# Kernel tuning notes

Hardware: AMD Instinct MI355X
Metric: run time of the kernel (lower is better)

The kernel has to match this reference:

```python
import jax, jax.numpy as jnp
import numpy as np
from jax import lax

EPS = 1e-5

def _conv(x, w, stride, padding):
    # x: NCHW, w: OIHW
    return lax.conv_general_dilated(
        x, w, window_strides=(stride, stride), padding=padding,
        dimension_numbers=("NCHW", "OIHW", "NCHW"))

def _bn(x, gamma, beta):
    # BatchNorm2d in training mode: batch statistics over (N, H, W)
    mean = jnp.mean(x, axis=(0, 2, 3), keepdims=True)
    var = jnp.var(x, axis=(0, 2, 3), keepdims=True)
    inv = lax.rsqrt(var + EPS)
    g = gamma.reshape(1, -1, 1, 1)
    b = beta.reshape(1, -1, 1, 1)
    return (x - mean) * inv * g + b

def setup_inputs() -> dict:
    key = jax.random.key(0)
    ks = jax.random.split(key, 5)
    B, Cin, H, W = 128, 64, 56, 56
    Cout = 128
    x = jax.random.normal(ks[0], (B, Cin, H, W), dtype=jnp.float32)
    w1 = jax.random.normal(ks[1], (Cout, Cin, 3, 3), dtype=jnp.float32) * 0.05
    w2 = jax.random.normal(ks[2], (Cout, Cout, 3, 3), dtype=jnp.float32) * 0.05
    wd = jax.random.normal(ks[3], (Cout, Cin, 1, 1), dtype=jnp.float32) * 0.05
    g1 = jnp.ones((Cout,), jnp.float32); b1 = jnp.zeros((Cout,), jnp.float32)
    g2 = jnp.ones((Cout,), jnp.float32); b2 = jnp.zeros((Cout,), jnp.float32)
    gd = jnp.ones((Cout,), jnp.float32); bd = jnp.zeros((Cout,), jnp.float32)
    return {"x": x, "w1": w1, "g1": g1, "b1": b1,
            "w2": w2, "g2": g2, "b2": b2,
            "wd": wd, "gd": gd, "bd": bd}

def reference(x, w1, g1, b1, w2, g2, b2, wd, gd, bd):
    stride = 2
    # conv1 (3x3, stride=2, 'same') -> BN -> ReLU
    out = _conv(x, w1, stride, "SAME")
    out = jax.nn.relu(_bn(out, g1, b1))
    # conv2 (3x3, stride=1, 'same') -> BN
    out = _conv(out, w2, 1, "SAME")
    out = _bn(out, g2, b2)
    # downsample identity: 1x1 conv stride=2 'valid' -> BN
    identity = _bn(_conv(x, wd, stride, "VALID"), gd, bd)
    return jax.nn.relu(out + identity)
```

## Files before the change

kernel.cpp:

```cpp
#include <hip/hip_runtime.h>

constexpr int B = 128, Cin = 64, H = 56, W = 56;
constexpr int Cout = 128, Ho = 28, Wo = 28;
constexpr int HW = Ho * Wo;
constexpr int NPIX = B * HW;
constexpr int NOUT = NPIX * Cout;
constexpr int NBLK2 = NPIX / 256;
constexpr float EPS_ = 1e-5f;
constexpr float CNT_ = (float)NPIX;

constexpr int HPX = 57, WPX = 57;
constexpr int HP1 = 30, WP1 = 30;

typedef __attribute__((ext_vector_type(8))) unsigned short u16x8;
typedef __attribute__((ext_vector_type(4))) unsigned short u16x4;
typedef __attribute__((ext_vector_type(8))) short bf16x8;
typedef __attribute__((ext_vector_type(4))) float f32x4;

__device__ inline float bf2f(unsigned short u) {
    union { unsigned int i; float f; } v; v.i = ((unsigned int)u) << 16; return v.f;
}
__device__ inline unsigned short f2bf(float f) {
    union { float f; unsigned int i; } v; v.f = f;
    return (unsigned short)((v.i + 0x7fffu + ((v.i >> 16) & 1u)) >> 16);
}

__device__ inline void gload16(const void* g, void* l) {
    __builtin_amdgcn_global_load_lds(
        (const __attribute__((address_space(1))) unsigned int*)g,
        (__attribute__((address_space(3))) unsigned int*)l, 16, 0, 0);
}

__global__ __launch_bounds__(512) void k_conv2_mfma(
        const unsigned short* __restrict__ xin,
        const unsigned short* __restrict__ wt,
        unsigned short* __restrict__ yout,
        float* __restrict__ part) {
    constexpr int CIN = 128, WP = 30, KTOT = 1152, NSTEP = 36;
    __shared__ unsigned short Alds[3][256 * 32];
    __shared__ unsigned short Blds[3][128 * 32];
    __shared__ float lsum[8][64], lsq[8][64];
    const int tid = threadIdx.x, w = tid >> 6, l = tid & 63;
    const int wr = w >> 1, wc = w & 1;
    const int bid = (blockIdx.x & 7) * (NBLK2 / 8) + (blockIdx.x >> 3);
    const int p0 = bid * 256;
    const char* xb = (const char*)xin;
    const char* wb = (const char*)wt;

    const int sslot = ((l & 3) ^ ((l >> 3) & 3)) * 16;
    const int rswz  = ((l >> 4) ^ ((l >> 1) & 3)) * 16;

    int gA[2], lofsA[2];
    #pragma unroll
    for (int i = 0; i < 2; ++i) {
        int row = w * 32 + i * 16 + (l >> 2);
        int p = p0 + row;
        int n = p / HW, rr = p % HW;
        int oh = rr / Wo, ow = rr % Wo;
        gA[i] = (((n * HP1 + oh) * WP + ow) * CIN) * 2 + sslot;
        lofsA[i] = row * 64 + (l & 3) * 16;
    }
    const int rowb = w * 16 + (l >> 2);
    const int gB = rowb * KTOT * 2 + sslot;
    const int lofsB = rowb * 64 + (l & 3) * 16;

    f32x4 acc[4][4];
    #pragma unroll
    for (int m = 0; m < 4; ++m)
        #pragma unroll
        for (int n = 0; n < 4; ++n)
            acc[m][n] = (f32x4){0.f, 0.f, 0.f, 0.f};

    gload16(xb + gA[0],      (char*)Alds[0] + lofsA[0]);
    gload16(xb + gA[1],      (char*)Alds[0] + lofsA[1]);
    gload16(wb + gB,         (char*)Blds[0] + lofsB);
    gload16(xb + gA[0] + 64, (char*)Alds[1] + lofsA[0]);
    gload16(xb + gA[1] + 64, (char*)Alds[1] + lofsA[1]);
    gload16(wb + gB + 64,    (char*)Blds[1] + lofsB);

    for (int oi = 0; oi < 3; ++oi) {
        const int Abase = oi * WP * CIN * 2;
        #pragma unroll
        for (int u = 0; u < 12; ++u) {
            const int s = oi * 12 + u;
            const int cur = u % 3;
            if (s + 1 < NSTEP) asm volatile("s_waitcnt vmcnt(3)" ::: "memory");
            else               asm volatile("s_waitcnt vmcnt(0)" ::: "memory");
            __builtin_amdgcn_s_barrier();
            if (s + 2 < NSTEP) {
                const int u2 = u + 2;
                const int j2 = u2 >> 2;
                const int c2 = u2 & 3;
                const int koffA = Abase + (j2 == 3 ? WP * CIN * 2 : j2 * CIN * 2) + c2 * 64;
                const int koffB = (s + 2) * 64;
                const int buf = u2 % 3;
                gload16(xb + gA[0] + koffA, (char*)Alds[buf] + lofsA[0]);
                gload16(xb + gA[1] + koffA, (char*)Alds[buf] + lofsA[1]);
                gload16(wb + gB + koffB,    (char*)Blds[buf] + lofsB);
            }
            bf16x8 bf[4];
            #pragma unroll
            for (int n = 0; n < 4; ++n)
                bf[n] = *(const bf16x8*)((const char*)Blds[cur] + (wc * 64 + n * 16 + (l & 15)) * 64 + rswz);
            #pragma unroll
            for (int m = 0; m < 4; ++m) {
                bf16x8 af = *(const bf16x8*)((const char*)Alds[cur] + (wr * 64 + m * 16 + (l & 15)) * 64 + rswz);
                #pragma unroll
                for (int n = 0; n < 4; ++n)
                    acc[m][n] = __builtin_amdgcn_mfma_f32_16x16x32_bf16(af, bf[n], acc[m][n], 0, 0, 0);
            }
        }
    }

    #pragma unroll
    for (int m = 0; m < 4; ++m) {
        int pq = p0 + wr * 64 + m * 16 + (l >> 4) * 4;
        int n = pq / HW, rr = pq % HW;
        #pragma unroll
        for (int q = 0; q < 4; ++q) {
            int co = wc * 64 + q * 16 + (l & 15);
            u16x4 v;
            #pragma unroll
            for (int r = 0; r < 4; ++r) v[r] = f2bf(acc[m][q][r]);
            *(u16x4*)(yout + ((size_t)(n * Cout + co)) * HW + rr) = v;
        }
    }

    float ps[4], pq_[4];
    #pragma unroll
    for (int n = 0; n < 4; ++n) {
        float s_ = 0.f, q_ = 0.f;
        #pragma unroll
        for (int m = 0; m < 4; ++m)
            #pragma unroll
            for (int r = 0; r < 4; ++r) { float v = acc[m][n][r]; s_ += v; q_ += v * v; }
        s_ += __shfl_xor(s_, 16); q_ += __shfl_xor(q_, 16);
        s_ += __shfl_xor(s_, 32); q_ += __shfl_xor(q_, 32);
        ps[n] = s_; pq_[n] = q_;
    }
    __syncthreads();
    if (l < 16) {
        #pragma unroll
        for (int n = 0; n < 4; ++n) { lsum[w][n * 16 + l] = ps[n]; lsq[w][n * 16 + l] = pq_[n]; }
    }
    __syncthreads();
    if (tid < 128) {
        int c = tid, half = c >> 6, j = c & 63;
        float s_ = 0.f, q_ = 0.f;
        #pragma unroll
        for (int r = 0; r < 4; ++r) { s_ += lsum[r * 2 + half][j]; q_ += lsq[r * 2 + half][j]; }
        part[((size_t)bid * 128 + c) * 2]     = s_;
        part[((size_t)bid * 128 + c) * 2 + 1] = q_;
    }
}

__global__ __launch_bounds__(512) void k_conv1_mfma(
        const unsigned short* __restrict__ xin,
        const unsigned short* __restrict__ wt,
        const unsigned short* __restrict__ wtd,
        unsigned short* __restrict__ yout,
        unsigned short* __restrict__ ydout,
        float* __restrict__ part, float* __restrict__ partd) {
    constexpr int CIN = 64, WP = 57, KTOT = 576, NSTEP = 18;
    __shared__ unsigned short Alds[3][256 * 32];
    __shared__ unsigned short Blds[3][128 * 32];
    __shared__ float lsum[8][64], lsq[8][64];
    const int tid = threadIdx.x, w = tid >> 6, l = tid & 63;
    const int wr = w >> 1, wc = w & 1;
    const int bid = (blockIdx.x & 7) * (NBLK2 / 8) + (blockIdx.x >> 3);
    const int p0 = bid * 256;
    const char* xb = (const char*)xin;
    const char* wb = (const char*)wt;

    const int sslot = ((l & 3) ^ ((l >> 3) & 3)) * 16;
    const int rswz  = ((l >> 4) ^ ((l >> 1) & 3)) * 16;

    int gA[2], lofsA[2];
    #pragma unroll
    for (int i = 0; i < 2; ++i) {
        int row = w * 32 + i * 16 + (l >> 2);
        int p = p0 + row;
        int n = p / HW, rr = p % HW;
        int oh = rr / Wo, ow = rr % Wo;
        gA[i] = (((n * HPX + oh * 2) * WP + ow * 2) * CIN) * 2 + sslot;
        lofsA[i] = row * 64 + (l & 3) * 16;
    }
    const int rowb = w * 16 + (l >> 2);
    const int gB = rowb * KTOT * 2 + sslot;
    const int lofsB = rowb * 64 + (l & 3) * 16;

    bf16x8 bd[2][4];
    #pragma unroll
    for (int s = 0; s < 2; ++s)
        #pragma unroll
        for (int n = 0; n < 4; ++n) {
            int co = wc * 64 + n * 16 + (l & 15);
            bd[s][n] = *(const bf16x8*)(wtd + co * 64 + s * 32 + (l >> 4) * 8);
        }

    f32x4 acc[4][4], accd[4][4];
    #pragma unroll
    for (int m = 0; m < 4; ++m)
        #pragma unroll
        for (int n = 0; n < 4; ++n) {
            acc[m][n]  = (f32x4){0.f, 0.f, 0.f, 0.f};
            accd[m][n] = (f32x4){0.f, 0.f, 0.f, 0.f};
        }

    #pragma unroll
    for (int s = 0; s < 2; ++s) {
        gload16(xb + gA[0] + s * 64, (char*)Alds[s] + lofsA[0]);
        gload16(xb + gA[1] + s * 64, (char*)Alds[s] + lofsA[1]);
        gload16(wb + gB + s * 64,    (char*)Blds[s] + lofsB);
    }

    #pragma unroll
    for (int s = 0; s < NSTEP; ++s) {
        const int cur = s % 3;
        if (s + 1 < NSTEP) asm volatile("s_waitcnt vmcnt(3)" ::: "memory");
        else               asm volatile("s_waitcnt vmcnt(0)" ::: "memory");
        __builtin_amdgcn_s_barrier();
        if (s + 2 < NSTEP) {
            const int s2 = s + 2;
            const int seg = s2 >> 1, kh = seg / 3, kw = seg % 3;
            const int koffA = (kh * WP + kw) * CIN * 2 + (s2 & 1) * 64;
            const int koffB = s2 * 64;
            const int buf = s2 % 3;
            gload16(xb + gA[0] + koffA, (char*)Alds[buf] + lofsA[0]);
            gload16(xb + gA[1] + koffA, (char*)Alds[buf] + lofsA[1]);
            gload16(wb + gB + koffB,    (char*)Blds[buf] + lofsB);
        }
        bf16x8 bf[4];
        #pragma unroll
        for (int n = 0; n < 4; ++n)
            bf[n] = *(const bf16x8*)((const char*)Blds[cur] + (wc * 64 + n * 16 + (l & 15)) * 64 + rswz);
        #pragma unroll
        for (int m = 0; m < 4; ++m) {
            bf16x8 af = *(const bf16x8*)((const char*)Alds[cur] + (wr * 64 + m * 16 + (l & 15)) * 64 + rswz);
            #pragma unroll
            for (int n = 0; n < 4; ++n)
                acc[m][n] = __builtin_amdgcn_mfma_f32_16x16x32_bf16(af, bf[n], acc[m][n], 0, 0, 0);
            if (s < 2) {
                #pragma unroll
                for (int n = 0; n < 4; ++n)
                    accd[m][n] = __builtin_amdgcn_mfma_f32_16x16x32_bf16(af, bd[s][n], accd[m][n], 0, 0, 0);
            }
        }
    }

    #pragma unroll
    for (int m = 0; m < 4; ++m) {
        #pragma unroll
        for (int r = 0; r < 4; ++r) {
            int p = p0 + wr * 64 + m * 16 + (l >> 4) * 4 + r;
            int n = p / HW, rr = p % HW;
            int oh = rr / Wo, ow = rr % Wo;
            unsigned short* dst = yout + ((size_t)((n * HP1 + oh + 1) * WP1 + ow + 1)) * 128
                                 + wc * 64 + (l & 15);
            #pragma unroll
            for (int q = 0; q < 4; ++q)
                dst[q * 16] = f2bf(acc[m][q][r]);
        }
    }
    #pragma unroll
    for (int m = 0; m < 4; ++m) {
        int pq = p0 + wr * 64 + m * 16 + (l >> 4) * 4;
        int n = pq / HW, rr = pq % HW;
        #pragma unroll
        for (int q = 0; q < 4; ++q) {
            int co = wc * 64 + q * 16 + (l & 15);
            u16x4 v;
            #pragma unroll
            for (int r = 0; r < 4; ++r) v[r] = f2bf(accd[m][q][r]);
            *(u16x4*)(ydout + ((size_t)(n * Cout + co)) * HW + rr) = v;
        }
    }

    #pragma unroll
    for (int pass = 0; pass < 2; ++pass) {
        f32x4 (&a)[4][4] = pass ? accd : acc;
        float* pt = pass ? partd : part;
        float ps[4], pq_[4];
        #pragma unroll
        for (int n = 0; n < 4; ++n) {
            float s_ = 0.f, q_ = 0.f;
            #pragma unroll
            for (int m = 0; m < 4; ++m)
                #pragma unroll
                for (int r = 0; r < 4; ++r) { float v = a[m][n][r]; s_ += v; q_ += v * v; }
            s_ += __shfl_xor(s_, 16); q_ += __shfl_xor(q_, 16);
            s_ += __shfl_xor(s_, 32); q_ += __shfl_xor(q_, 32);
            ps[n] = s_; pq_[n] = q_;
        }
        __syncthreads();
        if (l < 16) {
            #pragma unroll
            for (int n = 0; n < 4; ++n) { lsum[w][n * 16 + l] = ps[n]; lsq[w][n * 16 + l] = pq_[n]; }
        }
        __syncthreads();
        if (tid < 128) {
            int c = tid, half = c >> 6, j = c & 63;
            float s_ = 0.f, q_ = 0.f;
            #pragma unroll
            for (int r = 0; r < 4; ++r) { s_ += lsum[r * 2 + half][j]; q_ += lsq[r * 2 + half][j]; }
            pt[((size_t)bid * 128 + c) * 2]     = s_;
            pt[((size_t)bid * 128 + c) * 2 + 1] = q_;
        }
    }
}

constexpr int NZA = B * 113 * 8;
constexpr int NZB = B * 116 * 16;
constexpr int NWP = 73728 + 147456 + 8192;
__global__ __launch_bounds__(256) void k_prep(
        unsigned short* __restrict__ xb, unsigned short* __restrict__ y1p,
        const float* __restrict__ w1, const float* __restrict__ w2,
        const float* __restrict__ wd,
        unsigned short* __restrict__ wt1, unsigned short* __restrict__ wt2,
        unsigned short* __restrict__ wtd) {
    int idx = blockIdx.x * 256 + threadIdx.x;
    const u16x8 z = (u16x8){0, 0, 0, 0, 0, 0, 0, 0};
    if (idx < NZA) {
        int cg = idx & 7; int t = idx >> 3;
        int bp = t % 113, n = t / 113;
        int ih = bp < 57 ? 56 : bp - 57;
        int iw = bp < 57 ? bp : 56;
        *(u16x8*)(xb + ((size_t)((n * HPX + ih) * WPX + iw)) * Cin + cg * 8) = z;
    } else if (idx < NZA + NZB) {
        idx -= NZA;
        int cg = idx & 15; int t = idx >> 4;
        int bp = t % 116, n = t / 116;
        int oh, ow;
        if (bp < 30)      { oh = 0;           ow = bp; }
        else if (bp < 60) { oh = 29;          ow = bp - 30; }
        else if (bp < 88) { oh = bp - 60 + 1; ow = 0; }
        else              { oh = bp - 88 + 1; ow = 29; }
        *(u16x8*)(y1p + ((size_t)((n * HP1 + oh) * WP1 + ow)) * 128 + cg * 8) = z;
    } else {
        idx -= NZA + NZB;
        if (idx >= NWP) return;
        const float* w; unsigned short* wt; int cin, ntap;
        if (idx < 73728)               { w = w1; wt = wt1; cin = 64;  ntap = 9; }
        else if (idx < 73728 + 147456) { idx -= 73728; w = w2; wt = wt2; cin = 128; ntap = 9; }
        else                           { idx -= 73728 + 147456; w = wd; wt = wtd; cin = 64; ntap = 1; }
        int co = idx / (cin * ntap), r = idx % (cin * ntap);
        int ci = r / ntap, tap = r % ntap;
        wt[co * cin * ntap + tap * cin + ci] = f2bf(w[idx]);
    }
}

__global__ __launch_bounds__(512) void k_xprep(const float* __restrict__ x,
                                               unsigned short* __restrict__ xb) {
    __shared__ unsigned short lds[2][64 * 57];
    int n = blockIdx.x / (H / 2), ihp = blockIdx.x % (H / 2), ih0 = ihp * 2;
    const float* src = x + ((size_t)n * Cin * H + ih0) * W;
    for (int j = threadIdx.x; j < 2 * Cin * 14; j += 512) {
        int r = j / 896, rem = j % 896;
        int c = rem / 14, q = rem % 14;
        float4 v = *(const float4*)(src + ((size_t)c * H + r) * W + q * 4);
        unsigned short* d = &lds[r][c * 57 + q * 4];
        d[0] = f2bf(v.x); d[1] = f2bf(v.y); d[2] = f2bf(v.z); d[3] = f2bf(v.w);
    }
    __syncthreads();
    for (int k = threadIdx.x; k < 2 * W * 8; k += 512) {
        int r = k / 448, k2 = k % 448;
        int pix = k2 >> 3, cg = k2 & 7;
        u16x8 v;
        #pragma unroll
        for (int e = 0; e < 8; ++e) v[e] = lds[r][(cg * 8 + e) * 57 + pix];
        *(u16x8*)(xb + ((size_t)((n * HPX + ih0 + r) * WPX + pix)) * Cin + cg * 8) = v;
    }
}

__device__ inline void block_reduce2(float& s, float& s2) {
    #pragma unroll
    for (int off = 32; off > 0; off >>= 1) {
        s += __shfl_down(s, off);
        s2 += __shfl_down(s2, off);
    }
    __shared__ float ls[4], ls2[4];
    int wid = threadIdx.x >> 6, lane = threadIdx.x & 63;
    if (lane == 0) { ls[wid] = s; ls2[wid] = s2; }
    __syncthreads();
    if (threadIdx.x == 0) { s = ls[0] + ls[1] + ls[2] + ls[3]; s2 = ls2[0] + ls2[1] + ls2[2] + ls2[3]; }
}

__global__ __launch_bounds__(256) void k_finalize(
        const float* __restrict__ pA, const float* __restrict__ pB, int nA, int nB,
        const float* __restrict__ gA_, const float* __restrict__ bA_,
        const float* __restrict__ gB_, const float* __restrict__ bB_,
        float* __restrict__ scA, float* __restrict__ shA,
        float* __restrict__ scB, float* __restrict__ shB) {
    const bool second = blockIdx.x >= 128;
    const int c = blockIdx.x & 127;
    const float* part = second ? pB : pA;
    const int nblk = second ? nB : nA;
    const float* g = second ? gB_ : gA_;
    const float* b = second ? bB_ : bA_;
    float* scale = second ? scB : scA;
    float* shift = second ? shB : shA;
    float s = 0.f, q = 0.f;
    for (int k = threadIdx.x; k < nblk; k += 256) {
        s += part[((size_t)k * 128 + c) * 2];
        q += part[((size_t)k * 128 + c) * 2 + 1];
    }
    block_reduce2(s, q);
    if (threadIdx.x == 0) {
        float mean = s / CNT_;
        float var = q / CNT_ - mean * mean;
        float inv = rsqrtf(var + EPS_);
        scale[c] = g[c] * inv;
        shift[c] = b[c] - mean * g[c] * inv;
    }
}

__global__ __launch_bounds__(256) void k_bnrelu(unsigned short* __restrict__ y,
        const float* __restrict__ sc, const float* __restrict__ sh) {
    int t = threadIdx.x, cg = t & 7, pl = t >> 3;
    int p = blockIdx.x * 32 + pl;
    int n = p / HW, rr = p % HW;
    int oh = rr / Wo, ow = rr % Wo;
    size_t a = ((size_t)((n * HP1 + oh + 1) * WP1 + ow + 1)) * 128 + cg * 16;
    u16x8 v0 = *(u16x8*)(y + a);
    u16x8 v1 = *(u16x8*)(y + a + 8);
    u16x8 o0, o1;
    #pragma unroll
    for (int e = 0; e < 8; ++e) {
        float f0 = bf2f(v0[e]) * sc[cg * 16 + e] + sh[cg * 16 + e];
        float f1 = bf2f(v1[e]) * sc[cg * 16 + 8 + e] + sh[cg * 16 + 8 + e];
        o0[e] = f2bf(fmaxf(f0, 0.f));
        o1[e] = f2bf(fmaxf(f1, 0.f));
    }
    *(u16x8*)(y + a) = o0;
    *(u16x8*)(y + a + 8) = o1;
}

__global__ __launch_bounds__(256) void k_final(
        const unsigned short* __restrict__ y2, const unsigned short* __restrict__ yd,
        const float* __restrict__ sc2, const float* __restrict__ sh2,
        const float* __restrict__ scd, const float* __restrict__ shd,
        float* __restrict__ out) {
    int u = blockIdx.x * 256 + threadIdx.x;
    int plane = u / 49;
    int c = plane & (Cout - 1);
    int i = u % 49;
    size_t a = (size_t)plane * HW + i * 16;
    float s2c = sc2[c], h2c = sh2[c], sdc = scd[c], hdc = shd[c];
    #pragma unroll
    for (int hv = 0; hv < 2; ++hv) {
        u16x8 v2 = *(const u16x8*)(y2 + a + hv * 8);
        u16x8 vd = *(const u16x8*)(yd + a + hv * 8);
        float4 r0, r1;
        r0.x = fmaxf(bf2f(v2[0]) * s2c + h2c + bf2f(vd[0]) * sdc + hdc, 0.f);
        r0.y = fmaxf(bf2f(v2[1]) * s2c + h2c + bf2f(vd[1]) * sdc + hdc, 0.f);
        r0.z = fmaxf(bf2f(v2[2]) * s2c + h2c + bf2f(vd[2]) * sdc + hdc, 0.f);
        r0.w = fmaxf(bf2f(v2[3]) * s2c + h2c + bf2f(vd[3]) * sdc + hdc, 0.f);
        r1.x = fmaxf(bf2f(v2[4]) * s2c + h2c + bf2f(vd[4]) * sdc + hdc, 0.f);
        r1.y = fmaxf(bf2f(v2[5]) * s2c + h2c + bf2f(vd[5]) * sdc + hdc, 0.f);
        r1.z = fmaxf(bf2f(v2[6]) * s2c + h2c + bf2f(vd[6]) * sdc + hdc, 0.f);
        r1.w = fmaxf(bf2f(v2[7]) * s2c + h2c + bf2f(vd[7]) * sdc + hdc, 0.f);
        *(float4*)(out + a + hv * 8)     = r0;
        *(float4*)(out + a + hv * 8 + 4) = r1;
    }
}

extern "C" void kernel_launch(void* const* d_in, const int* in_sizes, int n_in,
                              void* d_out, int out_size, void* d_ws, size_t ws_size,
                              hipStream_t stream) {
    const float* x  = (const float*)d_in[0];
    const float* w1 = (const float*)d_in[1];
    const float* g1 = (const float*)d_in[2];
    const float* b1 = (const float*)d_in[3];
    const float* w2 = (const float*)d_in[4];
    const float* g2 = (const float*)d_in[5];
    const float* b2 = (const float*)d_in[6];
    const float* wd = (const float*)d_in[7];
    const float* gd = (const float*)d_in[8];
    const float* bd = (const float*)d_in[9];
    float* out = (float*)d_out;

    char* ws = (char*)d_ws;
    auto alloc = [&](size_t bytes) { char* p = ws; ws += (bytes + 255) & ~(size_t)255; return p; };
    unsigned short* xb  = (unsigned short*)alloc((size_t)B * HPX * WPX * Cin * 2);
    unsigned short* y1p = (unsigned short*)alloc((size_t)B * HP1 * WP1 * Cout * 2);
    unsigned short* y2b = (unsigned short*)alloc((size_t)NOUT * 2);
    unsigned short* ydb = (unsigned short*)alloc((size_t)NOUT * 2);
    unsigned short* wt1 = (unsigned short*)alloc((size_t)Cout * 576 * 2);
    unsigned short* wt2 = (unsigned short*)alloc((size_t)Cout * 1152 * 2);
    unsigned short* wtd = (unsigned short*)alloc((size_t)Cout * 64 * 2);
    float* part1 = (float*)alloc((size_t)NBLK2 * 128 * 2 * 4);
    float* part2 = (float*)alloc((size_t)NBLK2 * 128 * 2 * 4);
    float* partd = (float*)alloc((size_t)NBLK2 * 128 * 2 * 4);
    float* sc1 = (float*)alloc(128 * 4); float* sh1 = (float*)alloc(128 * 4);
    float* sc2 = (float*)alloc(128 * 4); float* sh2 = (float*)alloc(128 * 4);
    float* scd = (float*)alloc(128 * 4); float* shd = (float*)alloc(128 * 4);

    k_prep<<<(NZA + NZB + NWP + 255) / 256, 256, 0, stream>>>(
        xb, y1p, w1, w2, wd, wt1, wt2, wtd);
    k_xprep<<<B * (H / 2), 512, 0, stream>>>(x, xb);

    k_conv1_mfma<<<NBLK2, 512, 0, stream>>>(xb, wt1, wtd, y1p, ydb, part1, partd);

    k_finalize<<<128, 256, 0, stream>>>(part1, part1, NBLK2, NBLK2,
                                        g1, b1, g1, b1, sc1, sh1, sc1, sh1);
    k_bnrelu<<<NPIX / 32, 256, 0, stream>>>(y1p, sc1, sh1);

    k_conv2_mfma<<<NBLK2, 512, 0, stream>>>(y1p, wt2, y2b, part2);

    k_finalize<<<256, 256, 0, stream>>>(part2, partd, NBLK2, NBLK2,
                                        g2, b2, gd, bd, sc2, sh2, scd, shd);

    k_final<<<NOUT / 16 / 256, 256, 0, stream>>>(y2b, ydb, sc2, sh2, scd, shd, out);
}
```

Before: 172.1 us.

## Fuse conv2, BN2 statistics and final residual epilogue via cooperative grid sync

Turns conv2 into a cooperative kernel with 512-pixel tiles (196 blocks). Each block keeps its accumulators in registers, writes partial BN statistics, and after a grid sync the first blocks compute scale and shift per channel. After a second grid sync every block applies BN2, adds the BN-normalised downsample branch and applies ReLU straight from registers. This removes the bf16 y2 round trip through memory and two kernel launches. It also moves the downsample finalize to the first finalize call. The larger tile doubles the accumulator registers and LDS use, and with one block per CU occupancy could drop; the grid syncs add latency.

Result: slower. 205.3 us (+19.3%).

```diff
diff --git a/kernel.cpp b/kernel.cpp
--- a/kernel.cpp
+++ b/kernel.cpp
@@ -1,4 +1,6 @@
 #include <hip/hip_runtime.h>
+#include <hip/hip_cooperative_groups.h>
+namespace cg = cooperative_groups;
 
 constexpr int B = 128, Cin = 64, H = 56, W = 56;
 constexpr int Cout = 128, Ho = 28, Wo = 28;
@@ -6,6 +8,7 @@
 constexpr int NPIX = B * HW;
 constexpr int NOUT = NPIX * Cout;
 constexpr int NBLK2 = NPIX / 256;
+constexpr int NBLK3 = NPIX / 512;
 constexpr float EPS_ = 1e-5f;
 constexpr float CNT_ = (float)NPIX;
 
@@ -31,29 +34,32 @@
         (__attribute__((address_space(3))) unsigned int*)l, 16, 0, 0);
 }
 
-__global__ __launch_bounds__(512) void k_conv2_mfma(
+__global__ __launch_bounds__(512) void k_conv2f(
         const unsigned short* __restrict__ xin,
         const unsigned short* __restrict__ wt,
-        unsigned short* __restrict__ yout,
-        float* __restrict__ part) {
+        const unsigned short* __restrict__ ydb,
+        const float* __restrict__ g2, const float* __restrict__ b2,
+        const float* __restrict__ scd, const float* __restrict__ shd,
+        float* __restrict__ part2, float* __restrict__ sc2, float* __restrict__ sh2,
+        float* __restrict__ out) {
     constexpr int CIN = 128, WP = 30, KTOT = 1152, NSTEP = 36;
-    __shared__ unsigned short Alds[3][256 * 32];
+    __shared__ unsigned short Alds[3][512 * 32];
     __shared__ unsigned short Blds[3][128 * 32];
     __shared__ float lsum[8][64], lsq[8][64];
     const int tid = threadIdx.x, w = tid >> 6, l = tid & 63;
     const int wr = w >> 1, wc = w & 1;
-    const int bid = (blockIdx.x & 7) * (NBLK2 / 8) + (blockIdx.x >> 3);
-    const int p0 = bid * 256;
+    const int bid = blockIdx.x;
+    const int p0 = bid * 512;
     const char* xb = (const char*)xin;
     const char* wb = (const char*)wt;
 
     const int sslot = ((l & 3) ^ ((l >> 3) & 3)) * 16;
     const int rswz  = ((l >> 4) ^ ((l >> 1) & 3)) * 16;
 
-    int gA[2], lofsA[2];
-    #pragma unroll
-    for (int i = 0; i < 2; ++i) {
-        int row = w * 32 + i * 16 + (l >> 2);
+    int gA[4], lofsA[4];
+    #pragma unroll
+    for (int i = 0; i < 4; ++i) {
+        int row = w * 64 + i * 16 + (l >> 2);
         int p = p0 + row;
         int n = p / HW, rr = p % HW;
         int oh = rr / Wo, ow = rr % Wo;
@@ -64,19 +70,20 @@
     const int gB = rowb * KTOT * 2 + sslot;
     const int lofsB = rowb * 64 + (l & 3) * 16;
 
-    f32x4 acc[4][4];
-    #pragma unroll
-    for (int m = 0; m < 4; ++m)
+    f32x4 acc[8][4];
+    #pragma unroll
+    for (int m = 0; m < 8; ++m)
         #pragma unroll
         for (int n = 0; n < 4; ++n)
             acc[m][n] = (f32x4){0.f, 0.f, 0.f, 0.f};
 
-    gload16(xb + gA[0],      (char*)Alds[0] + lofsA[0]);
-    gload16(xb + gA[1],      (char*)Alds[0] + lofsA[1]);
-    gload16(wb + gB,         (char*)Blds[0] + lofsB);
-    gload16(xb + gA[0] + 64, (char*)Alds[1] + lofsA[0]);
-    gload16(xb + gA[1] + 64, (char*)Alds[1] + lofsA[1]);
-    gload16(wb + gB + 64,    (char*)Blds[1] + lofsB);
+    #pragma unroll
+    for (int s = 0; s < 2; ++s) {
+        #pragma unroll
+        for (int i = 0; i < 4; ++i)
+            gload16(xb + gA[i] + s * 64, (char*)Alds[s] + lofsA[i]);
+        gload16(wb + gB + s * 64, (char*)Blds[s] + lofsB);
+    }
 
     for (int oi = 0; oi < 3; ++oi) {
         const int Abase = oi * WP * CIN * 2;
@@ -84,7 +91,7 @@
         for (int u = 0; u < 12; ++u) {
             const int s = oi * 12 + u;
             const int cur = u % 3;
-            if (s + 1 < NSTEP) asm volatile("s_waitcnt vmcnt(3)" ::: "memory");
+            if (s + 1 < NSTEP) asm volatile("s_waitcnt vmcnt(5)" ::: "memory");
             else               asm volatile("s_waitcnt vmcnt(0)" ::: "memory");
             __builtin_amdgcn_s_barrier();
             if (s + 2 < NSTEP) {
@@ -94,17 +101,18 @@
                 const int koffA = Abase + (j2 == 3 ? WP * CIN * 2 : j2 * CIN * 2) + c2 * 64;
                 const int koffB = (s + 2) * 64;
                 const int buf = u2 % 3;
-                gload16(xb + gA[0] + koffA, (char*)Alds[buf] + lofsA[0]);
-                gload16(xb + gA[1] + koffA, (char*)Alds[buf] + lofsA[1]);
-                gload16(wb + gB + koffB,    (char*)Blds[buf] + lofsB);
+                #pragma unroll
+                for (int i = 0; i < 4; ++i)
+                    gload16(xb + gA[i] + koffA, (char*)Alds[buf] + lofsA[i]);
+                gload16(wb + gB + koffB, (char*)Blds[buf] + lofsB);
             }
             bf16x8 bf[4];
             #pragma unroll
             for (int n = 0; n < 4; ++n)
                 bf[n] = *(const bf16x8*)((const char*)Blds[cur] + (wc * 64 + n * 16 + (l & 15)) * 64 + rswz);
             #pragma unroll
-            for (int m = 0; m < 4; ++m) {
-                bf16x8 af = *(const bf16x8*)((const char*)Alds[cur] + (wr * 64 + m * 16 + (l & 15)) * 64 + rswz);
+            for (int m = 0; m < 8; ++m) {
+                bf16x8 af = *(const bf16x8*)((const char*)Alds[cur] + (wr * 128 + m * 16 + (l & 15)) * 64 + rswz);
                 #pragma unroll
                 for (int n = 0; n < 4; ++n)
                     acc[m][n] = __builtin_amdgcn_mfma_f32_16x16x32_bf16(af, bf[n], acc[m][n], 0, 0, 0);
@@ -112,45 +120,88 @@
         }
     }
 
-    #pragma unroll
-    for (int m = 0; m < 4; ++m) {
-        int pq = p0 + wr * 64 + m * 16 + (l >> 4) * 4;
+    {
+        float ps[4], pq_[4];
+        #pragma unroll
+        for (int n = 0; n < 4; ++n) {
+            float s_ = 0.f, q_ = 0.f;
+            #pragma unroll
+            for (int m = 0; m < 8; ++m)
+                #pragma unroll
+                for (int r = 0; r < 4; ++r) { float v = acc[m][n][r]; s_ += v; q_ += v * v; }
+            s_ += __shfl_xor(s_, 16); q_ += __shfl_xor(q_, 16);
+            s_ += __shfl_xor(s_, 32); q_ += __shfl_xor(q_, 32);
+            ps[n] = s_; pq_[n] = q_;
+        }
+        __syncthreads();
+        if (l < 16) {
+            #pragma unroll
+            for (int n = 0; n < 4; ++n) { lsum[w][n * 16 + l] = ps[n]; lsq[w][n * 16 + l] = pq_[n]; }
+        }
+        __syncthreads();
+        if (tid < 128) {
+            int c = tid, half = c >> 6, j = c & 63;
+            float s_ = 0.f, q_ = 0.f;
+            #pragma unroll
+            for (int r = 0; r < 4; ++r) { s_ += lsum[r * 2 + half][j]; q_ += lsq[r * 2 + half][j]; }
+            part2[((size_t)bid * 128 + c) * 2]     = s_;
+            part2[((size_t)bid * 128 + c) * 2 + 1] = q_;
+        }
+    }
+
+    cg::this_grid().sync();
+
+    if (bid < 128) {
+        const int c = bid;
+        float s_ = 0.f, q_ = 0.f;
+        if (tid < NBLK3) {
+            s_ = part2[((size_t)tid * 128 + c) * 2];
+            q_ = part2[((size_t)tid * 128 + c) * 2 + 1];
+        }
+        #pragma unroll
+        for (int off = 32; off > 0; off >>= 1) {
+            s_ += __shfl_down(s_, off);
+            q_ += __shfl_down(q_, off);
+        }
+        if (l == 0) { lsum[w][0] = s_; lsq[w][0] = q_; }
+        __syncthreads();
+        if (tid == 0) {
+            float S = 0.f, Q = 0.f;
+            #pragma unroll
+            for (int r = 0; r < 8; ++r) { S += lsum[r][0]; Q += lsq[r][0]; }
+            float mean = S / CNT_;
+            float var = Q / CNT_ - mean * mean;
+            float inv = rsqrtf(var + EPS_);
+            sc2[c] = g2[c] * inv;
+            sh2[c] = b2[c] - mean * g2[c] * inv;
+        }
+    }
+
+    cg::this_grid().sync();
+
+    float s2c[4], h2c[4], sdc[4], hdc[4];
+    #pragma unroll
+    for (int n = 0; n < 4; ++n) {
+        int co = wc * 64 + n * 16 + (l & 15);
+        s2c[n] = sc2[co]; h2c[n] = sh2[co];
+        sdc[n] = scd[co]; hdc[n] = shd[co];
+    }
+    #pragma unroll
+    for (int m = 0; m < 8; ++m) {
+        int pq = p0 + wr * 128 + m * 16 + (l >> 4) * 4;
         int n = pq / HW, rr = pq % HW;
         #pragma unroll
         for (int q = 0; q < 4; ++q) {
             int co = wc * 64 + q * 16 + (l & 15);
-            u16x4 v;
-            #pragma unroll
-            for (int r = 0; r < 4; ++r) v[r] = f2bf(acc[m][q][r]);
-            *(u16x4*)(yout + ((size_t)(n * Cout + co)) * HW + rr) = v;
-        }
-    }
-
-    float ps[4], pq_[4];
-    #pragma unroll
-    for (int n = 0; n < 4; ++n) {
-        float s_ = 0.f, q_ = 0.f;
-        #pragma unroll
-        for (int m = 0; m < 4; ++m)
-            #pragma unroll
-            for (int r = 0; r < 4; ++r) { float v = acc[m][n][r]; s_ += v; q_ += v * v; }
-        s_ += __shfl_xor(s_, 16); q_ += __shfl_xor(q_, 16);
-        s_ += __shfl_xor(s_, 32); q_ += __shfl_xor(q_, 32);
-        ps[n] = s_; pq_[n] = q_;
-    }
-    __syncthreads();
-    if (l < 16) {
-        #pragma unroll
-        for (int n = 0; n < 4; ++n) { lsum[w][n * 16 + l] = ps[n]; lsq[w][n * 16 + l] = pq_[n]; }
-    }
-    __syncthreads();
-    if (tid < 128) {
-        int c = tid, half = c >> 6, j = c & 63;
-        float s_ = 0.f, q_ = 0.f;
-        #pragma unroll
-        for (int r = 0; r < 4; ++r) { s_ += lsum[r * 2 + half][j]; q_ += lsq[r * 2 + half][j]; }
-        part[((size_t)bid * 128 + c) * 2]     = s_;
-        part[((size_t)bid * 128 + c) * 2 + 1] = q_;
+            size_t a = ((size_t)(n * Cout + co)) * HW + rr;
+            u16x4 vd = *(const u16x4*)(ydb + a);
+            float4 o;
+            o.x = fmaxf(acc[m][q][0] * s2c[q] + h2c[q] + bf2f(vd[0]) * sdc[q] + hdc[q], 0.f);
+            o.y = fmaxf(acc[m][q][1] * s2c[q] + h2c[q] + bf2f(vd[1]) * sdc[q] + hdc[q], 0.f);
+            o.z = fmaxf(acc[m][q][2] * s2c[q] + h2c[q] + bf2f(vd[2]) * sdc[q] + hdc[q], 0.f);
+            o.w = fmaxf(acc[m][q][3] * s2c[q] + h2c[q] + bf2f(vd[3]) * sdc[q] + hdc[q], 0.f);
+            *(float4*)(out + a) = o;
+        }
     }
 }
 
@@ -435,35 +486,6 @@
     *(u16x8*)(y + a + 8) = o1;
 }
 
-__global__ __launch_bounds__(256) void k_final(
-        const unsigned short* __restrict__ y2, const unsigned short* __restrict__ yd,
-        const float* __restrict__ sc2, const float* __restrict__ sh2,
-        const float* __restrict__ scd, const float* __restrict__ shd,
-        float* __restrict__ out) {
-    int u = blockIdx.x * 256 + threadIdx.x;
-    int plane = u / 49;
-    int c = plane & (Cout - 1);
-    int i = u % 49;
-    size_t a = (size_t)plane * HW + i * 16;
-    float s2c = sc2[c], h2c = sh2[c], sdc = scd[c], hdc = shd[c];
-    #pragma unroll
-    for (int hv = 0; hv < 2; ++hv) {
-        u16x8 v2 = *(const u16x8*)(y2 + a + hv * 8);
-        u16x8 vd = *(const u16x8*)(yd + a + hv * 8);
-        float4 r0, r1;
-        r0.x = fmaxf(bf2f(v2[0]) * s2c + h2c + bf2f(vd[0]) * sdc + hdc, 0.f);
-        r0.y = fmaxf(bf2f(v2[1]) * s2c + h2c + bf2f(vd[1]) * sdc + hdc, 0.f);
-        r0.z = fmaxf(bf2f(v2[2]) * s2c + h2c + bf2f(vd[2]) * sdc + hdc, 0.f);
-        r0.w = fmaxf(bf2f(v2[3]) * s2c + h2c + bf2f(vd[3]) * sdc + hdc, 0.f);
-        r1.x = fmaxf(bf2f(v2[4]) * s2c + h2c + bf2f(vd[4]) * sdc + hdc, 0.f);
-        r1.y = fmaxf(bf2f(v2[5]) * s2c + h2c + bf2f(vd[5]) * sdc + hdc, 0.f);
-        r1.z = fmaxf(bf2f(v2[6]) * s2c + h2c + bf2f(vd[6]) * sdc + hdc, 0.f);
-        r1.w = fmaxf(bf2f(v2[7]) * s2c + h2c + bf2f(vd[7]) * sdc + hdc, 0.f);
-        *(float4*)(out + a + hv * 8)     = r0;
-        *(float4*)(out + a + hv * 8 + 4) = r1;
-    }
-}
-
 extern "C" void kernel_launch(void* const* d_in, const int* in_sizes, int n_in,
                               void* d_out, int out_size, void* d_ws, size_t ws_size,
                               hipStream_t stream) {
@@ -483,13 +505,12 @@
     auto alloc = [&](size_t bytes) { char* p = ws; ws += (bytes + 255) & ~(size_t)255; return p; };
     unsigned short* xb  = (unsigned short*)alloc((size_t)B * HPX * WPX * Cin * 2);
     unsigned short* y1p = (unsigned short*)alloc((size_t)B * HP1 * WP1 * Cout * 2);
-    unsigned short* y2b = (unsigned short*)alloc((size_t)NOUT * 2);
     unsigned short* ydb = (unsigned short*)alloc((size_t)NOUT * 2);
     unsigned short* wt1 = (unsigned short*)alloc((size_t)Cout * 576 * 2);
     unsigned short* wt2 = (unsigned short*)alloc((size_t)Cout * 1152 * 2);
     unsigned short* wtd = (unsigned short*)alloc((size_t)Cout * 64 * 2);
     float* part1 = (float*)alloc((size_t)NBLK2 * 128 * 2 * 4);
-    float* part2 = (float*)alloc((size_t)NBLK2 * 128 * 2 * 4);
+    float* part2 = (float*)alloc((size_t)NBLK3 * 128 * 2 * 4);
     float* partd = (float*)alloc((size_t)NBLK2 * 128 * 2 * 4);
     float* sc1 = (float*)alloc(128 * 4); float* sh1 = (float*)alloc(128 * 4);
     float* sc2 = (float*)alloc(128 * 4); float* sh2 = (float*)alloc(128 * 4);
@@ -501,14 +522,22 @@
 
     k_conv1_mfma<<<NBLK2, 512, 0, stream>>>(xb, wt1, wtd, y1p, ydb, part1, partd);
 
-    k_finalize<<<128, 256, 0, stream>>>(part1, part1, NBLK2, NBLK2,
-                                        g1, b1, g1, b1, sc1, sh1, sc1, sh1);
+    k_finalize<<<256, 256, 0, stream>>>(part1, partd, NBLK2, NBLK2,
+                                        g1, b1, gd, bd, sc1, sh1, scd, shd);
     k_bnrelu<<<NPIX / 32, 256, 0, stream>>>(y1p, sc1, sh1);
 
-    k_conv2_mfma<<<NBLK2, 512, 0, stream>>>(y1p, wt2, y2b, part2);
-
-    k_finalize<<<256, 256, 0, stream>>>(part2, partd, NBLK2, NBLK2,
-                                        g2, b2, gd, bd, sc2, sh2, scd, shd);
-
-    k_final<<<NOUT / 16 / 256, 256, 0, stream>>>(y2b, ydb, sc2, sh2, scd, shd, out);
-}
+    {
+        const unsigned short* a_xin = y1p;
+        const unsigned short* a_wt  = wt2;
+        const unsigned short* a_yd  = ydb;
+        const float* a_g2 = g2; const float* a_b2 = b2;
+        const float* a_scd = scd; const float* a_shd = shd;
+        float* a_part2 = part2; float* a_sc2 = sc2; float* a_sh2 = sh2;
+        float* a_out = out;
+        void* args[] = {(void*)&a_xin, (void*)&a_wt, (void*)&a_yd,
+                        (void*)&a_g2, (void*)&a_b2, (void*)&a_scd, (void*)&a_shd,
+                        (void*)&a_part2, (void*)&a_sc2, (void*)&a_sh2, (void*)&a_out};
+        hipLaunchCooperativeKernel((void*)k_conv2f, dim3(NBLK3), dim3(512),
+                                   args, 0, stream);
+    }
+}
```
